# Performance work log

Hardware: AMD Instinct MI355X
Metric: run time of the kernel (lower is better)

The kernel has to match this reference:

```python
import jax, jax.numpy as jnp
import numpy as np


def setup_inputs() -> dict:
    key = jax.random.key(0)
    ks = jax.random.split(key, 6)
    B, C_in, C_out, H, W = 4, 256, 128, 64, 64
    return {
        "p": jax.random.normal(ks[0], (B, C_in, H, W), dtype=jnp.float32),
        "b": jax.random.normal(ks[1], (B, C_in, H, W), dtype=jnp.float32),
        "Wq": jax.random.normal(ks[2], (C_out, C_in), dtype=jnp.float32) * 0.05,
        "bq": jax.random.normal(ks[3], (C_out,), dtype=jnp.float32) * 0.05,
        "Wk": jax.random.normal(ks[4], (C_out, C_in), dtype=jnp.float32) * 0.05,
        "bk": jax.random.normal(ks[5], (C_out,), dtype=jnp.float32) * 0.05,
    }


def reference(p, b, Wq, bq, Wk, bk):
    # p, b: [B, C, H, W]; 1x1 convs are per-pixel GEMMs over channels.
    B, C, H, W = p.shape
    N = H * W
    p_flat = p.reshape(B, C, N)  # [B, C, N]
    b_flat = b.reshape(B, C, N)  # [B, C, N]
    # query = Conv1x1(p) -> [B, O, N] -> permuted to [B, N, O]
    q = jnp.einsum("bcn,oc->bno", p_flat, Wq) + bq  # [B, N, O]
    # key = Conv1x1(b) -> [B, O, N]
    k = jnp.einsum("bcn,oc->bon", b_flat, Wk) + bk[:, None]  # [B, O, N]
    energy = jnp.einsum("bno,bom->bnm", q, k)  # [B, N, N]
    attention = jax.nn.softmax(energy, axis=-1)
    # value = b flattened, attention applied over spatial tokens
    out = jnp.einsum("bnm,bcm->bcn", attention, b_flat)  # [B, C, N]
    return out.reshape(B, C, H, W)
```

## Files before the change

### kernel.cpp

```cpp
#include <hip/hip_runtime.h>
#include <stdint.h>


#define B_ 4
#define C_ 256
#define O_ 128
#define N_ 4096

#define AP 72
#define PP 40

typedef float v4f __attribute__((ext_vector_type(4)));
typedef short v8s __attribute__((ext_vector_type(8)));
typedef _Float16 v8h __attribute__((ext_vector_type(8)));
typedef uint32_t u32;
typedef unsigned short u16;

__device__ __forceinline__ u16 bf16_rne(float f) {
  u32 u = __builtin_bit_cast(u32, f);
  u += 0x7fffu + ((u >> 16) & 1u);
  return (u16)(u >> 16);
}
__device__ __forceinline__ float bf16_f(u16 s) {
  u32 u = ((u32)s) << 16;
  return __builtin_bit_cast(float, u);
}
__device__ __forceinline__ u16 f16_rne(float f) {
  _Float16 h = (_Float16)f;
  return __builtin_bit_cast(u16, h);
}
__device__ __forceinline__ float f16_f(u16 s) {
  return (float)__builtin_bit_cast(_Float16, s);
}
__device__ __forceinline__ v4f mfma16(v8s a, v8s b, v4f c) {
  return __builtin_amdgcn_mfma_f32_16x16x32_bf16(a, b, c, 0, 0, 0);
}
__device__ __forceinline__ v4f mfma16h(v8h a, v8h b, v4f c) {
  return __builtin_amdgcn_mfma_f32_16x16x32_f16(a, b, c, 0, 0, 0);
}
__device__ __forceinline__ void gl16(const u16* g, u16* l) {
  __builtin_amdgcn_global_load_lds(
      (const __attribute__((address_space(1))) u32*)g,
      (__attribute__((address_space(3))) u32*)l, 16, 0, 0);
}
template <int CTRL>
__device__ __forceinline__ float dppadd(float x) {
  int yi = __builtin_amdgcn_update_dpp(0, __builtin_bit_cast(int, x), CTRL,
                                       0xf, 0xf, true);
  return x + __builtin_bit_cast(float, yi);
}
__device__ __forceinline__ float sum16(float x) {
  x = dppadd<0xB1>(x);
  x = dppadd<0x4E>(x);
  x = dppadd<0x141>(x);
  x = dppadd<0x140>(x);
  return x;
}

__global__ __launch_bounds__(256) void k_wprep(const float* __restrict__ Wq,
                                               const float* __restrict__ Wk,
                                               u16* __restrict__ Wqh,
                                               u16* __restrict__ Wql,
                                               u16* __restrict__ Wkh,
                                               u16* __restrict__ Wkl) {
  const int inst = blockIdx.x >> 4;
  const float* src = inst ? Wk : Wq;
  u16* dh = inst ? Wkh : Wqh;
  u16* dl = inst ? Wkl : Wql;
  const int base = ((blockIdx.x & 15) * 256 + threadIdx.x) * 8;
  float4 a = ((const float4*)(src + base))[0];
  float4 c = ((const float4*)(src + base))[1];
  float v[8] = {a.x, a.y, a.z, a.w, c.x, c.y, c.z, c.w};
  u16 hh[8], ll[8];
#pragma unroll
  for (int j = 0; j < 8; j++) {
    hh[j] = bf16_rne(v[j]);
    ll[j] = bf16_rne(v[j] - bf16_f(hh[j]));
  }
  uint4 oh, ol;
  oh.x = (u32)hh[0] | ((u32)hh[1] << 16);
  oh.y = (u32)hh[2] | ((u32)hh[3] << 16);
  oh.z = (u32)hh[4] | ((u32)hh[5] << 16);
  oh.w = (u32)hh[6] | ((u32)hh[7] << 16);
  ol.x = (u32)ll[0] | ((u32)ll[1] << 16);
  ol.y = (u32)ll[2] | ((u32)ll[3] << 16);
  ol.z = (u32)ll[4] | ((u32)ll[5] << 16);
  ol.w = (u32)ll[6] | ((u32)ll[7] << 16);
  *(uint4*)(dh + base) = oh;
  *(uint4*)(dl + base) = ol;
}

__global__ __launch_bounds__(256, 4) void k_proj(
    const float* __restrict__ Xp, const float* __restrict__ Xb,
    const float* __restrict__ bq, const float* __restrict__ bk,
    const u16* __restrict__ Wqh, const u16* __restrict__ Wql,
    const u16* __restrict__ Wkh, const u16* __restrict__ Wkl,
    u16* __restrict__ Qh, u16* __restrict__ Ql, u16* __restrict__ Kh,
    u16* __restrict__ Vbf) {
  __shared__ __align__(16) short ah[32 * AP];
  __shared__ __align__(16) short al[32 * AP];
  const int tid = threadIdx.x;
  const int inst = blockIdx.x >> 9;
  const float* X = inst ? Xb : Xp;
  const u16* Wh = inst ? Wkh : Wqh;
  const u16* Wl = inst ? Wkl : Wql;
  const float* bias = inst ? bk : bq;
  const int b = (blockIdx.x >> 7) & 3;
  const int n0 = (blockIdx.x & 127) << 5;
  const int w = tid >> 6, lane = tid & 63, l15 = lane & 15, quad = lane >> 4;
  const int rg = w & 1;
  const int tq = w >> 1;
  v4f acc[4];
#pragma unroll
  for (int t = 0; t < 4; t++) acc[t] = (v4f){0.f, 0.f, 0.f, 0.f};

  const int sn = tid & 31;
  const int sg = tid >> 5;

  for (int c0 = 0; c0 < C_; c0 += 64) {
    __syncthreads();
    {
      const float* s = X + ((size_t)(b * C_ + c0 + sg * 8)) * N_ + n0 + sn;
      u16 hh[8], ll[8];
#pragma unroll
      for (int j = 0; j < 8; j++) {
        float v = s[(size_t)j * N_];
        hh[j] = bf16_rne(v);
        ll[j] = bf16_rne(v - bf16_f(hh[j]));
      }
      u32 ph[4], pl[4];
#pragma unroll
      for (int j = 0; j < 4; j++) {
        ph[j] = (u32)hh[2 * j] | ((u32)hh[2 * j + 1] << 16);
        pl[j] = (u32)ll[2 * j] | ((u32)ll[2 * j + 1] << 16);
      }
      *(uint4*)&ah[sn * AP + sg * 8] = make_uint4(ph[0], ph[1], ph[2], ph[3]);
      *(uint4*)&al[sn * AP + sg * 8] = make_uint4(pl[0], pl[1], pl[2], pl[3]);
      if (inst) {
#pragma unroll
        for (int j = 0; j < 8; j++)
          Vbf[((size_t)(b * C_ + c0 + sg * 8 + j)) * N_ + n0 + sn] = hh[j];
      }
    }
    __syncthreads();
#pragma unroll
    for (int s2 = 0; s2 < 2; s2++) {
      v8s a_h = *(const v8s*)&ah[(16 * rg + l15) * AP + 32 * s2 + 8 * quad];
      v8s a_l = *(const v8s*)&al[(16 * rg + l15) * AP + 32 * s2 + 8 * quad];
#pragma unroll
      for (int i = 0; i < 4; i++) {
        const size_t wo =
            (size_t)(16 * (4 * tq + i) + l15) * C_ + c0 + 32 * s2 + 8 * quad;
        v8s b_h = *(const v8s*)(Wh + wo);
        v8s b_l = *(const v8s*)(Wl + wo);
        acc[i] = mfma16(a_h, b_h, acc[i]);
        acc[i] = mfma16(a_h, b_l, acc[i]);
        acc[i] = mfma16(a_l, b_h, acc[i]);
      }
    }
  }
#pragma unroll
  for (int i = 0; i < 4; i++) {
    const int o = 16 * (4 * tq + i) + l15;
    const float bv = bias[o];
#pragma unroll
    for (int r = 0; r < 4; r++) {
      const int n = n0 + 16 * rg + 4 * quad + r;
      float v = acc[i][r] + bv;
      const size_t idx = (size_t)(b * N_ + n) * O_ + o;
      if (!inst) {
        u16 h = f16_rne(v);
        Qh[idx] = h;
        Ql[idx] = f16_rne(v - f16_f(h));
      } else {
        Kh[idx] = f16_rne(v);
      }
    }
  }
}

__global__ __launch_bounds__(256, 2) void k_flash(
    const u16* __restrict__ Qh, const u16* __restrict__ Ql,
    const u16* __restrict__ Khp, const u16* __restrict__ Vbf,
    u16* __restrict__ Opart, float* __restrict__ lpart) {
  __shared__ __align__(16) short smem[27136];
  short* Pt = smem + 24576;

  const int tid = threadIdx.x;
  const int w = tid >> 6, lane = tid & 63, l15 = lane & 15, quad = lane >> 4;
  const int h = blockIdx.x & 1;
  const int qt = (blockIdx.x >> 1) & 63;
  const int b = blockIdx.x >> 7;
  const int n0 = qt << 6;
  const int tok0 = h << 11;

  const u16* khb = Khp + (size_t)b * N_ * O_;
  const u16* vb = Vbf + (size_t)b * C_ * N_;
  short* pw = Pt + w * 16 * PP;

  v8h qh[4], ql[4];
  {
    const u16* qrh = Qh + (size_t)(b * N_ + n0 + 16 * w + l15) * O_;
    const u16* qrl = Ql + (size_t)(b * N_ + n0 + 16 * w + l15) * O_;
#pragma unroll
    for (int s = 0; s < 4; s++) {
      qh[s] = *(const v8h*)(qrh + 32 * s + 8 * quad);
      ql[s] = *(const v8h*)(qrl + 32 * s + 8 * quad);
    }
  }

  v4f oacc[16];
#pragma unroll
  for (int t = 0; t < 16; t++) oacc[t] = (v4f){0.f, 0.f, 0.f, 0.f};
  float lstate[4] = {0.f, 0.f, 0.f, 0.f};

  auto stage = [&](int mtn, int bi) {
    const int m0n = tok0 + (mtn << 5);
    short* kd = smem + bi * 12288;
    short* vd = kd + 4096;
#pragma unroll
    for (int i = 0; i < 2; i++) {
      const int R = 8 * w + 4 * i;
      const int rl = R + (lane >> 4);
      const int cg = (lane & 15) ^ (rl & 15);
      gl16(khb + ((size_t)(m0n + rl) << 7) + (cg << 3), (u16*)(kd + (R << 7)));
    }
#pragma unroll
    for (int i = 0; i < 4; i++) {
      const int R = 64 * w + 16 * i;
      const int rl = R + (lane >> 2);
      const int cg = (lane & 3) ^ ((rl >> 1) & 3);
      gl16(vb + (size_t)rl * N_ + m0n + (cg << 3), (u16*)(vd + (R << 5)));
    }
  };

  stage(0, 0);

#pragma unroll 1
  for (int mt = 0; mt < 64; mt++) {
    const int pr = mt & 1;
    __syncthreads();
    if (mt + 1 < 64) stage(mt + 1, 1 - pr);
    const short* kc = smem + pr * 12288;
    const short* vc = kc + 4096;

    v4f eh[2], el[2];
#pragma unroll
    for (int t = 0; t < 2; t++) {
      eh[t] = (v4f){0.f, 0.f, 0.f, 0.f};
      el[t] = (v4f){0.f, 0.f, 0.f, 0.f};
    }
#pragma unroll
    for (int s = 0; s < 4; s++) {
#pragma unroll
      for (int t = 0; t < 2; t++) {
        const int off = ((16 * t + l15) << 7) + (((4 * s + quad) ^ l15) << 3);
        const v8h kf = *(const v8h*)&kc[off];
        eh[t] = mfma16h(qh[s], kf, eh[t]);
        el[t] = mfma16h(ql[s], kf, el[t]);
      }
    }

#pragma unroll
    for (int r = 0; r < 4; r++) {
      float p0 = __expf(eh[0][r] + el[0][r]);
      float p1 = __expf(eh[1][r] + el[1][r]);
      lstate[r] += sum16(p0 + p1);
      pw[(4 * quad + r) * PP + l15] = (short)bf16_rne(p0);
      pw[(4 * quad + r) * PP + 16 + l15] = (short)bf16_rne(p1);
    }
    __builtin_amdgcn_s_waitcnt(0xC07F);
    asm volatile("s_barrier" ::: "memory");

    v8s af[4];
#pragma unroll
    for (int rw = 0; rw < 4; rw++)
      af[rw] = *(const v8s*)&Pt[(16 * rw + l15) * PP + 8 * quad];
#pragma unroll
    for (int cg = 0; cg < 4; cg++) {
      const int ch = 64 * w + 16 * cg + l15;
      const int voff = (ch << 5) + ((quad ^ ((ch >> 1) & 3)) << 3);
      const v8s vf = *(const v8s*)&vc[voff];
#pragma unroll
      for (int rw = 0; rw < 4; rw++)
        oacc[rw * 4 + cg] = mfma16(af[rw], vf, oacc[rw * 4 + cg]);
    }
  }

  __syncthreads();
  u16* outx = (u16*)smem;
#pragma unroll
  for (int rw = 0; rw < 4; rw++)
#pragma unroll
    for (int cg = 0; cg < 4; cg++) {
      const int ch = 64 * w + 16 * cg + l15;
      const v4f o = oacc[rw * 4 + cg];
      u32* q = (u32*)outx;
      const int base = ch * 36 + 8 * rw + 2 * quad;
      q[base] = (u32)bf16_rne(o[0]) | ((u32)bf16_rne(o[1]) << 16);
      q[base + 1] = (u32)bf16_rne(o[2]) | ((u32)bf16_rne(o[3]) << 16);
    }
  if (l15 == 0) {
#pragma unroll
    for (int r = 0; r < 4; r++)
      lpart[(size_t)blockIdx.x * 64 + 16 * w + 4 * quad + r] = lstate[r];
  }
  __syncthreads();
  {
    u16* od = Opart + (size_t)blockIdx.x * 16384;
    const int cr = tid >> 2, nch = (tid & 3) << 4;
#pragma unroll
    for (int it = 0; it < 4; it++) {
      const int c = cr + 64 * it;
      const u16* srcr = &outx[c * 72 + nch];
      uint4* dst = (uint4*)(od + c * 64 + nch);
      dst[0] = ((const uint4*)srcr)[0];
      dst[1] = ((const uint4*)srcr)[1];
    }
  }
}

__global__ __launch_bounds__(256) void k_merge(const u16* __restrict__ Opart,
                                               const float* __restrict__ lpart,
                                               float* __restrict__ out) {
  const int idx = blockIdx.x * 256 + threadIdx.x;
  const int e4 = idx << 2;
  const int b = e4 >> 20;
  const int c = (e4 >> 12) & 255;
  const int n = e4 & 4095;
  const int qt = n >> 6, row = n & 63;
  const int g = (b * 64 + qt) * 2;
  const u16* q0 = Opart + (size_t)g * 16384 + c * 64 + row;
  ushort4 a0 = *(const ushort4*)q0;
  ushort4 a1 = *(const ushort4*)(q0 + 16384);
  float4 l0 = *(const float4*)(lpart + (size_t)g * 64 + row);
  float4 l1 = *(const float4*)(lpart + (size_t)g * 64 + 64 + row);
  float4 o;
  o.x = (bf16_f(a0.x) + bf16_f(a1.x)) / (l0.x + l1.x);
  o.y = (bf16_f(a0.y) + bf16_f(a1.y)) / (l0.y + l1.y);
  o.z = (bf16_f(a0.z) + bf16_f(a1.z)) / (l0.z + l1.z);
  o.w = (bf16_f(a0.w) + bf16_f(a1.w)) / (l0.w + l1.w);
  *(float4*)(out + e4) = o;
}

extern "C" void kernel_launch(void* const* d_in, const int* in_sizes, int n_in,
                              void* d_out, int out_size, void* d_ws, size_t ws_size,
                              hipStream_t stream) {
  const float* p = (const float*)d_in[0];
  const float* bb = (const float*)d_in[1];
  const float* Wq = (const float*)d_in[2];
  const float* bq = (const float*)d_in[3];
  const float* Wk = (const float*)d_in[4];
  const float* bk = (const float*)d_in[5];
  float* out = (float*)d_out;

  const size_t plane = (size_t)B_ * N_ * O_;
  u16* Qh = (u16*)d_ws;
  u16* Ql = Qh + plane;
  u16* Kh = Ql + plane;
  u16* Vbf = Kh + plane;
  u16* Wqh = Vbf + 2 * plane;
  u16* Wql = Wqh + 32768;
  u16* Wkh = Wql + 32768;
  u16* Wkl = Wkh + 32768;
  u16* Opart = Wkl + 32768;
  float* lpart = (float*)(Opart + (size_t)512 * 16384);

  hipLaunchKernelGGL(k_wprep, dim3(32), dim3(256), 0, stream, Wq, Wk, Wqh, Wql,
                     Wkh, Wkl);
  hipLaunchKernelGGL(k_proj, dim3(1024), dim3(256), 0, stream, p, bb, bq, bk,
                     Wqh, Wql, Wkh, Wkl, Qh, Ql, Kh, Vbf);
  hipLaunchKernelGGL(k_flash, dim3(B_ * 64 * 2), dim3(256), 0, stream, Qh, Ql,
                     Kh, Vbf, Opart, lpart);
  hipLaunchKernelGGL(k_merge, dim3((B_ * C_ * N_) / (256 * 4)), dim3(256), 0,
                     stream, Opart, lpart, out);
}
```

Baseline: 207.2 us.

## Split flash attention key range three ways and defer row-sum reduction

Splits the key dimension across three blocks per query tile instead of two (42/42/44 tiles of 32 keys), giving 768 blocks so the grid fills the CUs better. Launch bounds go to three blocks per CU and the P tile pitch shrinks to cut LDS use. The per-iteration cross-lane row-sum reduction moves out of the loop into one reduction at the end. The merge kernel now reads three partials, which adds partial-output traffic, and the unpadded P pitch may cause LDS bank conflicts.

```diff
diff --git a/kernel.cpp b/kernel.cpp
--- a/kernel.cpp
+++ b/kernel.cpp
@@ -8,7 +8,7 @@
 #define N_ 4096
 
 #define AP 72
-#define PP 40
+#define PP 32
 
 typedef float v4f __attribute__((ext_vector_type(4)));
 typedef short v8s __attribute__((ext_vector_type(8)));
@@ -179,20 +179,22 @@
   }
 }
 
-__global__ __launch_bounds__(256, 2) void k_flash(
+__global__ __launch_bounds__(256, 3) void k_flash(
     const u16* __restrict__ Qh, const u16* __restrict__ Ql,
     const u16* __restrict__ Khp, const u16* __restrict__ Vbf,
     u16* __restrict__ Opart, float* __restrict__ lpart) {
-  __shared__ __align__(16) short smem[27136];
+  __shared__ __align__(16) short smem[26624];
   short* Pt = smem + 24576;
 
   const int tid = threadIdx.x;
   const int w = tid >> 6, lane = tid & 63, l15 = lane & 15, quad = lane >> 4;
-  const int h = blockIdx.x & 1;
-  const int qt = (blockIdx.x >> 1) & 63;
-  const int b = blockIdx.x >> 7;
+  const int bq = blockIdx.x / 3;
+  const int h = blockIdx.x - bq * 3;
+  const int qt = bq & 63;
+  const int b = bq >> 6;
   const int n0 = qt << 6;
-  const int tok0 = h << 11;
+  const int tok0 = h * 1344;
+  const int niter = (h == 2) ? 44 : 42;
 
   const u16* khb = Khp + (size_t)b * N_ * O_;
   const u16* vb = Vbf + (size_t)b * C_ * N_;
@@ -237,10 +239,10 @@
   stage(0, 0);
 
 #pragma unroll 1
-  for (int mt = 0; mt < 64; mt++) {
+  for (int mt = 0; mt < niter; mt++) {
     const int pr = mt & 1;
     __syncthreads();
-    if (mt + 1 < 64) stage(mt + 1, 1 - pr);
+    if (mt + 1 < niter) stage(mt + 1, 1 - pr);
     const short* kc = smem + pr * 12288;
     const short* vc = kc + 4096;
 
@@ -265,7 +267,7 @@
     for (int r = 0; r < 4; r++) {
       float p0 = __expf(eh[0][r] + el[0][r]);
       float p1 = __expf(eh[1][r] + el[1][r]);
-      lstate[r] += sum16(p0 + p1);
+      lstate[r] += p0 + p1;
       pw[(4 * quad + r) * PP + l15] = (short)bf16_rne(p0);
       pw[(4 * quad + r) * PP + 16 + l15] = (short)bf16_rne(p1);
     }
@@ -285,6 +287,15 @@
       for (int rw = 0; rw < 4; rw++)
         oacc[rw * 4 + cg] = mfma16(af[rw], vf, oacc[rw * 4 + cg]);
     }
+  }
+
+  float lsum[4];
+#pragma unroll
+  for (int r = 0; r < 4; r++) lsum[r] = sum16(lstate[r]);
+  if (l15 == 0) {
+#pragma unroll
+    for (int r = 0; r < 4; r++)
+      lpart[(size_t)blockIdx.x * 64 + 16 * w + 4 * quad + r] = lsum[r];
   }
 
   __syncthreads();
@@ -300,11 +311,6 @@
       q[base] = (u32)bf16_rne(o[0]) | ((u32)bf16_rne(o[1]) << 16);
       q[base + 1] = (u32)bf16_rne(o[2]) | ((u32)bf16_rne(o[3]) << 16);
     }
-  if (l15 == 0) {
-#pragma unroll
-    for (int r = 0; r < 4; r++)
-      lpart[(size_t)blockIdx.x * 64 + 16 * w + 4 * quad + r] = lstate[r];
-  }
   __syncthreads();
   {
     u16* od = Opart + (size_t)blockIdx.x * 16384;
@@ -329,17 +335,19 @@
   const int c = (e4 >> 12) & 255;
   const int n = e4 & 4095;
   const int qt = n >> 6, row = n & 63;
-  const int g = (b * 64 + qt) * 2;
+  const int g = (b * 64 + qt) * 3;
   const u16* q0 = Opart + (size_t)g * 16384 + c * 64 + row;
   ushort4 a0 = *(const ushort4*)q0;
   ushort4 a1 = *(const ushort4*)(q0 + 16384);
+  ushort4 a2 = *(const ushort4*)(q0 + 32768);
   float4 l0 = *(const float4*)(lpart + (size_t)g * 64 + row);
   float4 l1 = *(const float4*)(lpart + (size_t)g * 64 + 64 + row);
+  float4 l2 = *(const float4*)(lpart + (size_t)g * 64 + 128 + row);
   float4 o;
-  o.x = (bf16_f(a0.x) + bf16_f(a1.x)) / (l0.x + l1.x);
-  o.y = (bf16_f(a0.y) + bf16_f(a1.y)) / (l0.y + l1.y);
-  o.z = (bf16_f(a0.z) + bf16_f(a1.z)) / (l0.z + l1.z);
-  o.w = (bf16_f(a0.w) + bf16_f(a1.w)) / (l0.w + l1.w);
+  o.x = (bf16_f(a0.x) + bf16_f(a1.x) + bf16_f(a2.x)) / (l0.x + l1.x + l2.x);
+  o.y = (bf16_f(a0.y) + bf16_f(a1.y) + bf16_f(a2.y)) / (l0.y + l1.y + l2.y);
+  o.z = (bf16_f(a0.z) + bf16_f(a1.z) + bf16_f(a2.z)) / (l0.z + l1.z + l2.z);
+  o.w = (bf16_f(a0.w) + bf16_f(a1.w) + bf16_f(a2.w)) / (l0.w + l1.w + l2.w);
   *(float4*)(out + e4) = o;
 }
 
@@ -364,13 +372,13 @@
   u16* Wkh = Wql + 32768;
   u16* Wkl = Wkh + 32768;
   u16* Opart = Wkl + 32768;
-  float* lpart = (float*)(Opart + (size_t)512 * 16384);
+  float* lpart = (float*)(Opart + (size_t)768 * 16384);
 
   hipLaunchKernelGGL(k_wprep, dim3(32), dim3(256), 0, stream, Wq, Wk, Wqh, Wql,
                      Wkh, Wkl);
   hipLaunchKernelGGL(k_proj, dim3(1024), dim3(256), 0, stream, p, bb, bq, bk,
                      Wqh, Wql, Wkh, Wkl, Qh, Ql, Kh, Vbf);
-  hipLaunchKernelGGL(k_flash, dim3(B_ * 64 * 2), dim3(256), 0, stream, Qh, Ql,
+  hipLaunchKernelGGL(k_flash, dim3(B_ * 64 * 3), dim3(256), 0, stream, Qh, Ql,
                      Kh, Vbf, Opart, lpart);
   hipLaunchKernelGGL(k_merge, dim3((B_ * C_ * N_) / (256 * 4)), dim3(256), 0,
                      stream, Opart, lpart, out);
```

Result: faster. 202.5 us (-2.2%).
